# Optimization experiments

Hardware: AMD Instinct MI355X
Metric: run time of the kernel (lower is better)

Reference implementation:

```python
import jax, jax.numpy as jnp
import numpy as np

N_POINTS = 500000
GRID = 64          # D = H = W
C_VOX = 96         # voxel_feat_dim
C_PT = 32          # point_feat_dim
OFF_DIM = (C_VOX + C_PT) // 2          # 64
DEC_DIM = C_VOX + C_PT + OFF_DIM       # 192


def setup_inputs() -> dict:
    key = jax.random.key(0)
    ks = jax.random.split(key, 10)
    return {
        "voxel_feat": jax.random.normal(ks[0], (C_VOX, GRID, GRID, GRID), jnp.float32),
        "voxel_coords": jax.random.randint(ks[1], (N_POINTS, 3), 0, GRID, jnp.int32),
        "point_feat": jax.random.normal(ks[2], (N_POINTS, C_PT), jnp.float32),
        "point_offsets": jax.random.normal(ks[3], (N_POINTS, 3), jnp.float32),
        # offset_encoder: Linear(3, OFF_DIM), stored as [in, out]
        "W_off": jax.random.normal(ks[4], (3, OFF_DIM), jnp.float32) * 0.1,
        "b_off": jax.random.normal(ks[5], (OFF_DIM,), jnp.float32) * 0.1,
        # decoder MLP: Linear(DEC_DIM, DEC_DIM//2) -> GELU -> Linear(DEC_DIM//2, 3)
        "W1": jax.random.normal(ks[6], (DEC_DIM, DEC_DIM // 2), jnp.float32) * 0.1,
        "b1": jax.random.normal(ks[7], (DEC_DIM // 2,), jnp.float32) * 0.1,
        "W2": jax.random.normal(ks[8], (DEC_DIM // 2, 3), jnp.float32) * 0.1,
        "b2": jax.random.normal(ks[9], (3,), jnp.float32) * 0.1,
    }


def reference(voxel_feat, voxel_coords, point_feat, point_offsets,
              W_off, b_off, W1, b1, W2, b2):
    # Irregular voxel-to-point gather: voxel_feat[:, z, y, x].T -> [N, C_VOX]
    z, y, x = voxel_coords[:, 2], voxel_coords[:, 1], voxel_coords[:, 0]
    voxel_to_point_feat = voxel_feat[:, z, y, x].T  # [N, C_VOX]

    concated = jnp.concatenate([point_feat, voxel_to_point_feat], axis=-1)  # [N, 128]
    offsets_feature = point_offsets @ W_off + b_off                          # [N, 64]
    feat = jnp.concatenate([concated, offsets_feature], axis=-1)            # [N, 192]

    h = jax.nn.gelu(feat @ W1 + b1, approximate=False)  # torch nn.GELU is exact erf
    flow = h @ W2 + b2                                   # [N, 3]
    return flow
```

## Files before the change

kernel.cpp:

```cpp
#include <hip/hip_runtime.h>
#include <math.h>

#define NPTS   500000
#define GRIDW  64
#define NVOX   (GRIDW*GRIDW*GRIDW)
#define C_VOXC 96
#define C_PTC  32
#define OFFD   64
#define HID    96
#define HHALF  48

__device__ __forceinline__ unsigned f2bf(float f) {
    unsigned u = __float_as_uint(f);
    unsigned r = u + 0x7fffu + ((u >> 16) & 1u);
    return r >> 16;
}
__device__ __forceinline__ float bflo(unsigned u) {
    return __uint_as_float(u << 16);
}
__device__ __forceinline__ float bfhi(unsigned u) {
    return __uint_as_float(u & 0xffff0000u);
}

__device__ __forceinline__ float gelu_fast(float s) {
    const float u  = s * 0.70710678118654752440f;
    const float au = fabsf(u);
    const float t  = __fdividef(1.0f, fmaf(0.3275911f, au, 1.0f));
    float p = fmaf(1.061405429f, t, -1.453152027f);
    p = fmaf(p, t, 1.421413741f);
    p = fmaf(p, t, -0.284496736f);
    p = fmaf(p, t, 0.254829592f);
    p *= t;
    const float e = __expf(-u * u);
    float r = fmaf(-p, e, 1.0f);
    r = copysignf(r, u);
    return 0.5f * s * (1.0f + r);
}

__global__ void fold_kernel(const float* __restrict__ W_off,
                            const float* __restrict__ b_off,
                            const float* __restrict__ W1,
                            const float* __restrict__ b1,
                            float* __restrict__ Wc,
                            float* __restrict__ bcomb) {
    int j = threadIdx.x;
    if (j >= HID) return;
    float bc = b1[j];
    float w0 = 0.f, w1 = 0.f, w2 = 0.f;
    for (int d = 0; d < OFFD; ++d) {
        float w = W1[(C_PTC + C_VOXC + d) * HID + j];
        bc += b_off[d] * w;
        w0 = fmaf(W_off[0 * OFFD + d], w, w0);
        w1 = fmaf(W_off[1 * OFFD + d], w, w1);
        w2 = fmaf(W_off[2 * OFFD + d], w, w2);
    }
    Wc[0 * HID + j] = w0;
    Wc[1 * HID + j] = w1;
    Wc[2 * HID + j] = w2;
    bcomb[j] = bc;
}

__global__ __launch_bounds__(256, 8) void voxgemm_kernel(
        const float* __restrict__ vf,
        const float* __restrict__ W1,
        uint4* __restrict__ vc) {
    const int tid = threadIdx.x;
    const int tv  = tid & 63;
    const int tj  = __builtin_amdgcn_readfirstlane(tid >> 6);
    const int v   = blockIdx.x * 64 + tv;
    const int j0  = tj * 24;
    const float* __restrict__ Wv = W1 + C_PTC * HID + j0;

    float acc[24];
#pragma unroll
    for (int jj = 0; jj < 24; ++jj) acc[jj] = 0.f;

#pragma unroll 4
    for (int c = 0; c < C_VOXC; ++c) {
        const float a = vf[(size_t)c * NVOX + v];
        const float* __restrict__ wr = Wv + c * HID;
#pragma unroll
        for (int jj = 0; jj < 24; ++jj)
            acc[jj] = fmaf(a, wr[jj], acc[jj]);
    }

    uint4* __restrict__ d4 = vc + (size_t)v * 12 + tj * 3;
#pragma unroll
    for (int k = 0; k < 3; ++k) {
        const int j = k * 8;
        unsigned a0 = f2bf(acc[j + 0]) | (f2bf(acc[j + 1]) << 16);
        unsigned a1 = f2bf(acc[j + 2]) | (f2bf(acc[j + 3]) << 16);
        unsigned a2 = f2bf(acc[j + 4]) | (f2bf(acc[j + 5]) << 16);
        unsigned a3 = f2bf(acc[j + 6]) | (f2bf(acc[j + 7]) << 16);
        d4[k] = make_uint4(a0, a1, a2, a3);
    }
}

__global__ __launch_bounds__(256, 4) void point_kernel(
        const int* __restrict__ coords,
        const float* __restrict__ pf,
        const float* __restrict__ po,
        const float* __restrict__ W1,
        const float* __restrict__ W2,
        const float* __restrict__ b2,
        const float* __restrict__ Wc,
        const float* __restrict__ bcomb,
        const uint4* __restrict__ vc,
        float* __restrict__ out) {
    const int i = blockIdx.x * 256 + threadIdx.x;
    if (i >= NPTS) return;

    const int x = coords[i * 3 + 0];
    const int y = coords[i * 3 + 1];
    const int z = coords[i * 3 + 2];
    const int vidx = (z * GRIDW + y) * GRIDW + x;
    const uint4* __restrict__ vrow = vc + (size_t)vidx * 12;

    const float o0 = po[i * 3 + 0];
    const float o1 = po[i * 3 + 1];
    const float o2 = po[i * 3 + 2];
    const float4* __restrict__ pf4 =
        reinterpret_cast<const float4*>(pf + (size_t)i * C_PTC);

    float f0 = b2[0], f1 = b2[1], f2 = b2[2];

#pragma unroll
    for (int h = 0; h < 2; ++h) {
        const int j0 = h * HHALF;

        uint4 vr[6];
#pragma unroll
        for (int q = 0; q < 6; ++q) vr[q] = vrow[h * 6 + q];

        float acc[HHALF];
#pragma unroll
        for (int j = 0; j < HHALF; ++j) {
            float a = fmaf(o2, Wc[2 * HID + j0 + j], bcomb[j0 + j]);
            a = fmaf(o1, Wc[1 * HID + j0 + j], a);
            acc[j] = fmaf(o0, Wc[0 * HID + j0 + j], a);
        }

#pragma unroll 2
        for (int kk = 0; kk < 8; ++kk) {
            const float4 p = pf4[kk];
            const float pv[4] = {p.x, p.y, p.z, p.w};
#pragma unroll
            for (int t = 0; t < 4; ++t) {
                const float* __restrict__ wr = W1 + (kk * 4 + t) * HID + j0;
#pragma unroll
                for (int j = 0; j < HHALF; ++j)
                    acc[j] = fmaf(pv[t], wr[j], acc[j]);
            }
        }

#pragma unroll
        for (int q = 0; q < 6; ++q) {
            const unsigned a0 = vr[q].x, a1 = vr[q].y,
                           a2 = vr[q].z, a3 = vr[q].w;
            acc[8 * q + 0] += bflo(a0);
            acc[8 * q + 1] += bfhi(a0);
            acc[8 * q + 2] += bflo(a1);
            acc[8 * q + 3] += bfhi(a1);
            acc[8 * q + 4] += bflo(a2);
            acc[8 * q + 5] += bfhi(a2);
            acc[8 * q + 6] += bflo(a3);
            acc[8 * q + 7] += bfhi(a3);
        }

#pragma unroll
        for (int j = 0; j < HHALF; ++j) {
            const float hh = gelu_fast(acc[j]);
            f0 = fmaf(hh, W2[(j0 + j) * 3 + 0], f0);
            f1 = fmaf(hh, W2[(j0 + j) * 3 + 1], f1);
            f2 = fmaf(hh, W2[(j0 + j) * 3 + 2], f2);
        }
    }

    out[i * 3 + 0] = f0;
    out[i * 3 + 1] = f1;
    out[i * 3 + 2] = f2;
}

__global__ __launch_bounds__(256) void point_direct_kernel(
        const int* __restrict__ coords,
        const float* __restrict__ vf,
        const float* __restrict__ pf,
        const float* __restrict__ po,
        const float* __restrict__ W1,
        const float* __restrict__ W2,
        const float* __restrict__ b2,
        const float* __restrict__ Wc,
        const float* __restrict__ bcomb,
        float* __restrict__ out) {
    const int i = blockIdx.x * 256 + threadIdx.x;
    if (i >= NPTS) return;

    const int x = coords[i * 3 + 0];
    const int y = coords[i * 3 + 1];
    const int z = coords[i * 3 + 2];
    const int vidx = (z * GRIDW + y) * GRIDW + x;

    float acc[HID];
#pragma unroll
    for (int j = 0; j < HID; ++j) acc[j] = bcomb[j];

    const float* __restrict__ W1v = W1 + C_PTC * HID;
    for (int c = 0; c < C_VOXC; ++c) {
        const float a = vf[(size_t)c * NVOX + vidx];
#pragma unroll
        for (int j = 0; j < HID; ++j)
            acc[j] = fmaf(a, W1v[c * HID + j], acc[j]);
    }

    const float o0 = po[i * 3 + 0];
    const float o1 = po[i * 3 + 1];
    const float o2 = po[i * 3 + 2];
#pragma unroll
    for (int j = 0; j < HID; ++j) {
        float a = fmaf(o2, Wc[2 * HID + j], acc[j]);
        a = fmaf(o1, Wc[1 * HID + j], a);
        acc[j] = fmaf(o0, Wc[0 * HID + j], a);
    }

    const float* __restrict__ pfr = pf + (size_t)i * C_PTC;
    for (int k = 0; k < C_PTC; ++k) {
        const float fk = pfr[k];
#pragma unroll
        for (int j = 0; j < HID; ++j)
            acc[j] = fmaf(fk, W1[k * HID + j], acc[j]);
    }

    float f0 = b2[0], f1 = b2[1], f2 = b2[2];
#pragma unroll
    for (int j = 0; j < HID; ++j) {
        const float hh = gelu_fast(acc[j]);
        f0 = fmaf(hh, W2[j * 3 + 0], f0);
        f1 = fmaf(hh, W2[j * 3 + 1], f1);
        f2 = fmaf(hh, W2[j * 3 + 2], f2);
    }

    out[i * 3 + 0] = f0;
    out[i * 3 + 1] = f1;
    out[i * 3 + 2] = f2;
}

extern "C" void kernel_launch(void* const* d_in, const int* in_sizes, int n_in,
                              void* d_out, int out_size, void* d_ws, size_t ws_size,
                              hipStream_t stream) {
    const float* vf    = (const float*)d_in[0];
    const int*   vcrd  = (const int*)  d_in[1];
    const float* pf    = (const float*)d_in[2];
    const float* po    = (const float*)d_in[3];
    const float* W_off = (const float*)d_in[4];
    const float* b_off = (const float*)d_in[5];
    const float* W1    = (const float*)d_in[6];
    const float* b1    = (const float*)d_in[7];
    const float* W2    = (const float*)d_in[8];
    const float* b2    = (const float*)d_in[9];
    float* out = (float*)d_out;

    float* Wc    = (float*)d_ws;
    float* bcomb = Wc + 384;
    uint4* vcb   = reinterpret_cast<uint4*>((char*)d_ws + 4096);

    const size_t need = 4096 + (size_t)NVOX * HID * sizeof(unsigned short);

    fold_kernel<<<1, 128, 0, stream>>>(W_off, b_off, W1, b1, Wc, bcomb);

    if (ws_size >= need) {
        voxgemm_kernel<<<NVOX / 64, 256, 0, stream>>>(vf, W1, vcb);
        point_kernel<<<(NPTS + 255) / 256, 256, 0, stream>>>(
            vcrd, pf, po, W1, W2, b2, Wc, bcomb, vcb, out);
    } else {
        point_direct_kernel<<<(NPTS + 255) / 256, 256, 0, stream>>>(
            vcrd, vf, pf, po, W1, W2, b2, Wc, bcomb, out);
    }
}
```

Baseline: 389.9 us.

## Split hidden units across four waves per point block with LDS reduction

Restructures point_kernel so each 256-thread block handles 64 points, with each of the four waves computing a 24-wide slice of the 96 hidden units for the same points. Point features are staged through shared memory with coalesced loads, and the partial W2 outputs are reduced across waves via LDS. This cuts per-thread register pressure (24 accumulators instead of 48) so occupancy can rise, and it makes the weight index wave-uniform for scalar loads. In exchange it adds two barriers, LDS traffic and a serial reduction done only by wave 0.

```diff
diff --git a/kernel.cpp b/kernel.cpp
--- a/kernel.cpp
+++ b/kernel.cpp
@@ -8,7 +8,6 @@
 #define C_PTC  32
 #define OFFD   64
 #define HID    96
-#define HHALF  48
 
 __device__ __forceinline__ unsigned f2bf(float f) {
     unsigned u = __float_as_uint(f);
@@ -96,7 +95,7 @@
     }
 }
 
-__global__ __launch_bounds__(256, 4) void point_kernel(
+__global__ __launch_bounds__(256, 8) void point_kernel(
         const int* __restrict__ coords,
         const float* __restrict__ pf,
         const float* __restrict__ po,
@@ -107,78 +106,115 @@
         const float* __restrict__ bcomb,
         const uint4* __restrict__ vc,
         float* __restrict__ out) {
-    const int i = blockIdx.x * 256 + threadIdx.x;
-    if (i >= NPTS) return;
-
-    const int x = coords[i * 3 + 0];
-    const int y = coords[i * 3 + 1];
-    const int z = coords[i * 3 + 2];
-    const int vidx = (z * GRIDW + y) * GRIDW + x;
-    const uint4* __restrict__ vrow = vc + (size_t)vidx * 12;
-
-    const float o0 = po[i * 3 + 0];
-    const float o1 = po[i * 3 + 1];
-    const float o2 = po[i * 3 + 2];
-    const float4* __restrict__ pf4 =
-        reinterpret_cast<const float4*>(pf + (size_t)i * C_PTC);
-
-    float f0 = b2[0], f1 = b2[1], f2 = b2[2];
-
-#pragma unroll
-    for (int h = 0; h < 2; ++h) {
-        const int j0 = h * HHALF;
-
-        uint4 vr[6];
-#pragma unroll
-        for (int q = 0; q < 6; ++q) vr[q] = vrow[h * 6 + q];
-
-        float acc[HHALF];
-#pragma unroll
-        for (int j = 0; j < HHALF; ++j) {
-            float a = fmaf(o2, Wc[2 * HID + j0 + j], bcomb[j0 + j]);
-            a = fmaf(o1, Wc[1 * HID + j0 + j], a);
-            acc[j] = fmaf(o0, Wc[0 * HID + j0 + j], a);
+    __shared__ float pf_s[64][33];
+    __shared__ float part[4][64][3];
+
+    const int tid  = threadIdx.x;
+    const int lane = tid & 63;
+    const int w    = tid >> 6;
+    const int wj   = __builtin_amdgcn_readfirstlane(w);
+    const int p0   = blockIdx.x * 64;
+    const int p    = p0 + lane;
+    const bool valid = (p < NPTS);
+
+    {
+        const int r  = tid >> 2;
+        const int c0 = (tid & 3) * 8;
+        const int pp = p0 + r;
+        float v[8];
+        if (pp < NPTS) {
+            const float4* __restrict__ src =
+                reinterpret_cast<const float4*>(pf + (size_t)pp * C_PTC + c0);
+            float4 u0 = src[0], u1 = src[1];
+            v[0]=u0.x; v[1]=u0.y; v[2]=u0.z; v[3]=u0.w;
+            v[4]=u1.x; v[5]=u1.y; v[6]=u1.z; v[7]=u1.w;
+        } else {
+#pragma unroll
+            for (int t = 0; t < 8; ++t) v[t] = 0.f;
         }
-
-#pragma unroll 2
-        for (int kk = 0; kk < 8; ++kk) {
-            const float4 p = pf4[kk];
-            const float pv[4] = {p.x, p.y, p.z, p.w};
-#pragma unroll
-            for (int t = 0; t < 4; ++t) {
-                const float* __restrict__ wr = W1 + (kk * 4 + t) * HID + j0;
-#pragma unroll
-                for (int j = 0; j < HHALF; ++j)
-                    acc[j] = fmaf(pv[t], wr[j], acc[j]);
-            }
-        }
-
-#pragma unroll
-        for (int q = 0; q < 6; ++q) {
-            const unsigned a0 = vr[q].x, a1 = vr[q].y,
-                           a2 = vr[q].z, a3 = vr[q].w;
-            acc[8 * q + 0] += bflo(a0);
-            acc[8 * q + 1] += bfhi(a0);
-            acc[8 * q + 2] += bflo(a1);
-            acc[8 * q + 3] += bfhi(a1);
-            acc[8 * q + 4] += bflo(a2);
-            acc[8 * q + 5] += bfhi(a2);
-            acc[8 * q + 6] += bflo(a3);
-            acc[8 * q + 7] += bfhi(a3);
-        }
-
-#pragma unroll
-        for (int j = 0; j < HHALF; ++j) {
-            const float hh = gelu_fast(acc[j]);
-            f0 = fmaf(hh, W2[(j0 + j) * 3 + 0], f0);
-            f1 = fmaf(hh, W2[(j0 + j) * 3 + 1], f1);
-            f2 = fmaf(hh, W2[(j0 + j) * 3 + 2], f2);
-        }
-    }
-
-    out[i * 3 + 0] = f0;
-    out[i * 3 + 1] = f1;
-    out[i * 3 + 2] = f2;
+#pragma unroll
+        for (int t = 0; t < 8; ++t) pf_s[r][c0 + t] = v[t];
+    }
+
+    int vidx = 0;
+    float o0 = 0.f, o1 = 0.f, o2 = 0.f;
+    uint4 vr0 = make_uint4(0,0,0,0), vr1 = vr0, vr2 = vr0;
+    if (valid) {
+        const int x = coords[p * 3 + 0];
+        const int y = coords[p * 3 + 1];
+        const int z = coords[p * 3 + 2];
+        vidx = (z * GRIDW + y) * GRIDW + x;
+        const uint4* __restrict__ vrow = vc + (size_t)vidx * 12 + wj * 3;
+        vr0 = vrow[0]; vr1 = vrow[1]; vr2 = vrow[2];
+        o0 = po[p * 3 + 0];
+        o1 = po[p * 3 + 1];
+        o2 = po[p * 3 + 2];
+    }
+
+    __syncthreads();
+
+    const int j0 = wj * 24;
+
+    float acc[24];
+#pragma unroll
+    for (int jj = 0; jj < 24; ++jj) {
+        float a = fmaf(o2, Wc[2 * HID + j0 + jj], bcomb[j0 + jj]);
+        a = fmaf(o1, Wc[1 * HID + j0 + jj], a);
+        acc[jj] = fmaf(o0, Wc[0 * HID + j0 + jj], a);
+    }
+
+#pragma unroll
+    for (int k = 0; k < C_PTC; ++k) {
+        const float s = pf_s[lane][k];
+        const float* __restrict__ wr = W1 + k * HID + j0;
+#pragma unroll
+        for (int jj = 0; jj < 24; ++jj)
+            acc[jj] = fmaf(s, wr[jj], acc[jj]);
+    }
+
+    {
+        const unsigned a0 = vr0.x, a1 = vr0.y, a2 = vr0.z, a3 = vr0.w;
+        acc[0] += bflo(a0);  acc[1] += bfhi(a0);
+        acc[2] += bflo(a1);  acc[3] += bfhi(a1);
+        acc[4] += bflo(a2);  acc[5] += bfhi(a2);
+        acc[6] += bflo(a3);  acc[7] += bfhi(a3);
+        const unsigned b0 = vr1.x, b1_ = vr1.y, b2_ = vr1.z, b3 = vr1.w;
+        acc[8]  += bflo(b0);  acc[9]  += bfhi(b0);
+        acc[10] += bflo(b1_); acc[11] += bfhi(b1_);
+        acc[12] += bflo(b2_); acc[13] += bfhi(b2_);
+        acc[14] += bflo(b3);  acc[15] += bfhi(b3);
+        const unsigned c0 = vr2.x, c1 = vr2.y, c2 = vr2.z, c3 = vr2.w;
+        acc[16] += bflo(c0);  acc[17] += bfhi(c0);
+        acc[18] += bflo(c1);  acc[19] += bfhi(c1);
+        acc[20] += bflo(c2);  acc[21] += bfhi(c2);
+        acc[22] += bflo(c3);  acc[23] += bfhi(c3);
+    }
+
+    float f0 = 0.f, f1 = 0.f, f2 = 0.f;
+#pragma unroll
+    for (int jj = 0; jj < 24; ++jj) {
+        const float hh = gelu_fast(acc[jj]);
+        f0 = fmaf(hh, W2[(j0 + jj) * 3 + 0], f0);
+        f1 = fmaf(hh, W2[(j0 + jj) * 3 + 1], f1);
+        f2 = fmaf(hh, W2[(j0 + jj) * 3 + 2], f2);
+    }
+    part[wj][lane][0] = f0;
+    part[wj][lane][1] = f1;
+    part[wj][lane][2] = f2;
+
+    __syncthreads();
+
+    if (w == 0 && valid) {
+        const float r0 = part[0][lane][0] + part[1][lane][0] +
+                         part[2][lane][0] + part[3][lane][0] + b2[0];
+        const float r1 = part[0][lane][1] + part[1][lane][1] +
+                         part[2][lane][1] + part[3][lane][1] + b2[1];
+        const float r2 = part[0][lane][2] + part[1][lane][2] +
+                         part[2][lane][2] + part[3][lane][2] + b2[2];
+        out[p * 3 + 0] = r0;
+        out[p * 3 + 1] = r1;
+        out[p * 3 + 2] = r2;
+    }
 }
 
 __global__ __launch_bounds__(256) void point_direct_kernel(
@@ -269,7 +305,7 @@
 
     if (ws_size >= need) {
         voxgemm_kernel<<<NVOX / 64, 256, 0, stream>>>(vf, W1, vcb);
-        point_kernel<<<(NPTS + 255) / 256, 256, 0, stream>>>(
+        point_kernel<<<(NPTS + 63) / 64, 256, 0, stream>>>(
             vcrd, pf, po, W1, W2, b2, Wc, bcomb, vcb, out);
     } else {
         point_direct_kernel<<<(NPTS + 255) / 256, 256, 0, stream>>>(
```

Measured after the change: 329.1 us. 1.18x faster.
